# Performance work log

Hardware: AMD Instinct MI355X
Metric: run time of the kernel (lower is better)

## Reference

```python
import jax, jax.numpy as jnp
import numpy as np

BATCH, N_STEPS, STATE_DIM = 8192, 128, 16
HIDDEN = 50
IN0 = STATE_DIM + 1  # features + prev_delta


def _lstm_cell(x, h, c, w_ih, w_hh, b):
    # PyTorch gate order: i, f, g, o
    gates = x @ w_ih.T + h @ w_hh.T + b  # (B, 4H)
    i, f, g, o = jnp.split(gates, 4, axis=-1)
    c_new = jax.nn.sigmoid(f) * c + jax.nn.sigmoid(i) * jnp.tanh(g)
    h_new = jax.nn.sigmoid(o) * jnp.tanh(c_new)
    return h_new, c_new


def setup_inputs() -> dict:
    key = jax.random.key(0)
    ks = jax.random.split(key, 8)
    s = 0.1
    return {
        "features": jax.random.normal(ks[0], (BATCH, N_STEPS, STATE_DIM), dtype=jnp.float32),
        "w_ih0": jax.random.normal(ks[1], (4 * HIDDEN, IN0), dtype=jnp.float32) * s,
        "w_hh0": jax.random.normal(ks[2], (4 * HIDDEN, HIDDEN), dtype=jnp.float32) * s,
        "b_0": jnp.zeros((4 * HIDDEN,), dtype=jnp.float32),  # bias_ih + bias_hh (both init to 0)
        "w_ih1": jax.random.normal(ks[3], (4 * HIDDEN, HIDDEN), dtype=jnp.float32) * s,
        "w_hh1": jax.random.normal(ks[4], (4 * HIDDEN, HIDDEN), dtype=jnp.float32) * s,
        "b_1": jnp.zeros((4 * HIDDEN,), dtype=jnp.float32),
        "w_fc1": jax.random.normal(ks[5], (HIDDEN // 2, HIDDEN), dtype=jnp.float32) * s,
        "b_fc1": jnp.zeros((HIDDEN // 2,), dtype=jnp.float32),
        "w_fc2": jax.random.normal(ks[6], (1, HIDDEN // 2), dtype=jnp.float32) * s,
        "b_fc2": jnp.zeros((1,), dtype=jnp.float32),
    }


def reference(features, w_ih0, w_hh0, b_0, w_ih1, w_hh1, b_1, w_fc1, b_fc1, w_fc2, b_fc2):
    B = features.shape[0]
    feats_t = jnp.swapaxes(features, 0, 1)  # (T, B, state_dim)
    z = jnp.zeros((B, HIDDEN), dtype=features.dtype)
    init = (z, z, z, z, jnp.zeros((B, 1), dtype=features.dtype))

    def step(carry, x_t):
        h0, c0, h1, c1, prev_delta = carry
        x = jnp.concatenate([x_t, prev_delta], axis=-1)  # (B, state_dim+1)
        h0, c0 = _lstm_cell(x, h0, c0, w_ih0, w_hh0, b_0)
        h1, c1 = _lstm_cell(h0, h1, c1, w_ih1, w_hh1, b_1)
        delta = jax.nn.relu(h1 @ w_fc1.T + b_fc1) @ w_fc2.T + b_fc2  # (B, 1)
        return (h0, c0, h1, c1, delta), delta[:, 0]

    _, deltas = jax.lax.scan(step, init, feats_t)  # (T, B)
    return jnp.swapaxes(deltas, 0, 1)  # (B, T)
```

## Files before the change

### kernel.cpp

```cpp
#include <hip/hip_runtime.h>
#include <math.h>

#define BATCH    8192
#define TSTEPS   128
#define SDIM     16
#define HID      50
#define IN0      17
#define BT       16
#define NTHREADS 256

#define K0P 72
#define K1P 104
#define KFP 64

typedef _Float16 half_t;
typedef __attribute__((ext_vector_type(8))) _Float16 half8;
typedef __attribute__((ext_vector_type(4))) float    floatx4;

#define MFMA16(a, b, c) __builtin_amdgcn_mfma_f32_16x16x32_f16((a), (b), (c), 0, 0, 0)

__device__ __forceinline__ float sig_u(float x) {
    float e = __expf(-x);
    return __builtin_amdgcn_rcpf(1.0f + e);
}
__device__ __forceinline__ float tanh_u(float x) {
    float e = __expf(-2.0f * x);
    return fmaf(2.0f, __builtin_amdgcn_rcpf(1.0f + e), -1.0f);
}
__device__ __forceinline__ void hsplit(float v, half_t* hp, half_t* lp) {
    half_t h = (half_t)v;
    *hp = h;
    *lp = (half_t)(v - (float)h);
}

__global__ __launch_bounds__(NTHREADS, 2)
void lstm2_mfma_regw_kernel(const float* __restrict__ feat,
                            const float* __restrict__ w_ih0,
                            const float* __restrict__ w_hh0,
                            const float* __restrict__ b_0,
                            const float* __restrict__ w_ih1,
                            const float* __restrict__ w_hh1,
                            const float* __restrict__ b_1,
                            const float* __restrict__ w_fc1,
                            const float* __restrict__ b_fc1,
                            const float* __restrict__ w_fc2,
                            const float* __restrict__ b_fc2,
                            float* __restrict__ out)
{
    __shared__ __align__(16) half_t smW[200 * K1P];
    __shared__ __align__(16) half_t X0h[BT * K0P], X0l[BT * K0P];
    __shared__ __align__(16) half_t X1h[BT * K1P], X1l[BT * K1P];

    const int tid  = threadIdx.x;
    const int lane = tid & 63;
    const int wv   = tid >> 6;
    const int quad = lane >> 4;
    const int col  = lane & 15;
    const int b0   = blockIdx.x * BT;

    const int tstart = wv * 3 + (wv == 3 ? 1 : 0);
    const int tcnt   = 3 + (wv == 2 ? 1 : 0);

    const half8 hz = {0, 0, 0, 0, 0, 0, 0, 0};


    for (int i = tid; i < 200 * K0P; i += NTHREADS) {
        int row = i / K0P, k = i - row * K0P;
        int j = row >> 2, q = row & 3, orig = q * HID + j;
        float v = 0.0f;
        if (k < IN0)            v = w_ih0[orig * IN0 + k];
        else if (k < IN0 + HID) v = w_hh0[orig * HID + (k - IN0)];
        smW[i] = (half_t)v;
    }
    __syncthreads();
    half8 a0f[3][4];
    #pragma unroll
    for (int kt = 0; kt < 3; ++kt) {
        int k0 = 32 * kt + quad * 8;
        #pragma unroll
        for (int ti = 0; ti < 4; ++ti) {
            a0f[kt][ti] = hz;
            int row = 16 * (tstart + ti) + col;
            if (ti < tcnt && row < 200 && k0 < K0P)
                a0f[kt][ti] = *(const half8*)(smW + row * K0P + k0);
        }
    }
    __syncthreads();

    for (int i = tid; i < 200 * K1P; i += NTHREADS) {
        int row = i / K1P, k = i - row * K1P;
        int j = row >> 2, q = row & 3, orig = q * HID + j;
        float v = 0.0f;
        if (k < HID)                      v = w_hh1[orig * HID + k];
        else if (k >= 52 && k < 52 + HID) v = w_ih1[orig * HID + (k - 52)];
        smW[i] = (half_t)v;
    }
    __syncthreads();
    half8 a1f[4][4];
    #pragma unroll
    for (int kt = 0; kt < 4; ++kt) {
        int k0 = 32 * kt + quad * 8;
        #pragma unroll
        for (int ti = 0; ti < 4; ++ti) {
            a1f[kt][ti] = hz;
            int row = 16 * (tstart + ti) + col;
            if (ti < tcnt && row < 200 && k0 < K1P)
                a1f[kt][ti] = *(const half8*)(smW + row * K1P + k0);
        }
    }
    __syncthreads();

    for (int i = tid; i < 32 * KFP; i += NTHREADS) {
        int row = i >> 6, k = i & 63;
        smW[i] = (half_t)((row < 25 && k < HID) ? w_fc1[row * HID + k] : 0.0f);
    }
    for (int i = tid; i < BT * K0P; i += NTHREADS) { X0h[i] = (half_t)0.0f; X0l[i] = (half_t)0.0f; }
    for (int i = tid; i < BT * K1P; i += NTHREADS) { X1h[i] = (half_t)0.0f; X1l[i] = (half_t)0.0f; }
    __syncthreads();

    half8 wff[2][2];
    wff[0][0] = hz; wff[0][1] = hz; wff[1][0] = hz; wff[1][1] = hz;
    if (wv == 0) {
        #pragma unroll
        for (int kt = 0; kt < 2; ++kt) {
            int k0 = 32 * kt + quad * 8;
            #pragma unroll
            for (int tf = 0; tf < 2; ++tf) {
                int row = 16 * tf + col;
                wff[kt][tf] = *(const half8*)(smW + row * KFP + k0);
            }
        }
    }

    const int xs = tid >> 4, xk = tid & 15;
    const size_t fbase = (size_t)(b0 + xs) * (TSTEPS * SDIM) + xk;
    hsplit(feat[fbase], &X0h[xs * K0P + xk], &X0l[xs * K0P + xk]);

    floatx4 bias0[4], bias1[4];
    #pragma unroll
    for (int ti = 0; ti < 4; ++ti) {
        floatx4 z = {0.f, 0.f, 0.f, 0.f};
        bias0[ti] = z; bias1[ti] = z;
        int u = 4 * (tstart + ti) + quad;
        if (ti < tcnt && u < HID) {
            bias0[ti][0] = b_0[u];           bias0[ti][1] = b_0[HID + u];
            bias0[ti][2] = b_0[2 * HID + u]; bias0[ti][3] = b_0[3 * HID + u];
            bias1[ti][0] = b_1[u];           bias1[ti][1] = b_1[HID + u];
            bias1[ti][2] = b_1[2 * HID + u]; bias1[ti][3] = b_1[3 * HID + u];
        }
    }
    floatx4 w2r[2], bfr[2];
    { floatx4 z = {0.f, 0.f, 0.f, 0.f}; w2r[0] = z; w2r[1] = z; bfr[0] = z; bfr[1] = z; }
    float bf2 = 0.0f;
    if (wv == 0) {
        bf2 = b_fc2[0];
        #pragma unroll
        for (int tf = 0; tf < 2; ++tf)
            #pragma unroll
            for (int r5 = 0; r5 < 4; ++r5) {
                int r = 16 * tf + quad * 4 + r5;
                if (r < 25) { w2r[tf][r5] = w_fc2[r]; bfr[tf][r5] = b_fc1[r]; }
            }
    }

    float c0s[4] = {0.f, 0.f, 0.f, 0.f};
    float c1s[4] = {0.f, 0.f, 0.f, 0.f};
    __syncthreads();

    for (int t = 0; t < TSTEPS; ++t) {
        float fnext = (t + 1 < TSTEPS) ? feat[fbase + (size_t)(t + 1) * SDIM] : 0.0f;

        floatx4 acc[4];
        #pragma unroll
        for (int ti = 0; ti < 4; ++ti) acc[ti] = bias0[ti];
        #pragma unroll
        for (int kt = 0; kt < 3; ++kt) {
            int k0 = 32 * kt + quad * 8;
            half8 bh = hz, bl = hz;
            if (k0 < K0P) {
                bh = *(const half8*)(X0h + col * K0P + k0);
                bl = *(const half8*)(X0l + col * K0P + k0);
            }
            #pragma unroll
            for (int ti = 0; ti < 4; ++ti) {
                if (ti < tcnt) {
                    acc[ti] = MFMA16(a0f[kt][ti], bh, acc[ti]);
                    acc[ti] = MFMA16(a0f[kt][ti], bl, acc[ti]);
                }
            }
        }
        __syncthreads();

        #pragma unroll
        for (int ti = 0; ti < 4; ++ti) {
            if (ti < tcnt) {
                int u = 4 * (tstart + ti) + quad;
                float i_ = sig_u(acc[ti][0]);
                float f_ = sig_u(acc[ti][1]);
                float g_ = tanh_u(acc[ti][2]);
                float o_ = sig_u(acc[ti][3]);
                float c  = f_ * c0s[ti] + i_ * g_;
                c0s[ti]  = c;
                float h  = o_ * tanh_u(c);
                half_t hh, hl;
                hsplit(h, &hh, &hl);
                X1h[col * K1P + 52 + u] = hh;  X1l[col * K1P + 52 + u] = hl;
                X0h[col * K0P + IN0 + u] = hh; X0l[col * K0P + IN0 + u] = hl;
            }
        }
        __syncthreads();

        floatx4 acc1[4];
        #pragma unroll
        for (int ti = 0; ti < 4; ++ti) acc1[ti] = bias1[ti];
        #pragma unroll
        for (int kt = 0; kt < 4; ++kt) {
            int k0 = 32 * kt + quad * 8;
            half8 bh = hz, bl = hz;
            if (k0 < K1P) {
                bh = *(const half8*)(X1h + col * K1P + k0);
                bl = *(const half8*)(X1l + col * K1P + k0);
            }
            #pragma unroll
            for (int ti = 0; ti < 4; ++ti) {
                if (ti < tcnt) {
                    acc1[ti] = MFMA16(a1f[kt][ti], bh, acc1[ti]);
                    acc1[ti] = MFMA16(a1f[kt][ti], bl, acc1[ti]);
                }
            }
        }
        __syncthreads();

        #pragma unroll
        for (int ti = 0; ti < 4; ++ti) {
            if (ti < tcnt) {
                int u = 4 * (tstart + ti) + quad;
                float i_ = sig_u(acc1[ti][0]);
                float f_ = sig_u(acc1[ti][1]);
                float g_ = tanh_u(acc1[ti][2]);
                float o_ = sig_u(acc1[ti][3]);
                float c  = f_ * c1s[ti] + i_ * g_;
                c1s[ti]  = c;
                float h  = o_ * tanh_u(c);
                half_t hh, hl;
                hsplit(h, &hh, &hl);
                X1h[col * K1P + u] = hh;  X1l[col * K1P + u] = hl;
            }
        }
        __syncthreads();

        if (wv == 0) {
            floatx4 accf[2];
            accf[0] = bfr[0]; accf[1] = bfr[1];
            #pragma unroll
            for (int kt = 0; kt < 2; ++kt) {
                int k0 = 32 * kt + quad * 8;
                half8 bh = *(const half8*)(X1h + col * K1P + k0);
                half8 bl = *(const half8*)(X1l + col * K1P + k0);
                #pragma unroll
                for (int tf = 0; tf < 2; ++tf) {
                    accf[tf] = MFMA16(wff[kt][tf], bh, accf[tf]);
                    accf[tf] = MFMA16(wff[kt][tf], bl, accf[tf]);
                }
            }
            float p = 0.0f;
            #pragma unroll
            for (int tf = 0; tf < 2; ++tf)
                #pragma unroll
                for (int r5 = 0; r5 < 4; ++r5)
                    p += w2r[tf][r5] * fmaxf(accf[tf][r5], 0.0f);
            p += __shfl_xor(p, 16);
            p += __shfl_xor(p, 32);
            float d = p + bf2;
            if (lane < 16) {
                out[(size_t)(b0 + lane) * TSTEPS + t] = d;
                hsplit(d, &X0h[lane * K0P + 16], &X0l[lane * K0P + 16]);
            }
        }
        if (t + 1 < TSTEPS)
            hsplit(fnext, &X0h[xs * K0P + xk], &X0l[xs * K0P + xk]);
        __syncthreads();
    }
}

extern "C" void kernel_launch(void* const* d_in, const int* in_sizes, int n_in,
                              void* d_out, int out_size, void* d_ws, size_t ws_size,
                              hipStream_t stream) {
    const float* feat  = (const float*)d_in[0];
    const float* w_ih0 = (const float*)d_in[1];
    const float* w_hh0 = (const float*)d_in[2];
    const float* b_0   = (const float*)d_in[3];
    const float* w_ih1 = (const float*)d_in[4];
    const float* w_hh1 = (const float*)d_in[5];
    const float* b_1   = (const float*)d_in[6];
    const float* w_fc1 = (const float*)d_in[7];
    const float* b_fc1 = (const float*)d_in[8];
    const float* w_fc2 = (const float*)d_in[9];
    const float* b_fc2 = (const float*)d_in[10];
    float* out = (float*)d_out;

    dim3 grid(BATCH / BT);
    dim3 block(NTHREADS);
    hipLaunchKernelGGL(lstm2_mfma_regw_kernel, grid, block, 0, stream,
                       feat, w_ih0, w_hh0, b_0, w_ih1, w_hh1, b_1,
                       w_fc1, b_fc1, w_fc2, b_fc2, out);
}
```

Baseline: 480.1 us.

## Double-buffer LSTM activations, reuse layer-0 h in registers, drop two barriers per step

Replaces the separate X0/X1 activation tiles with one unified, ping-ponged row layout holding features, delta, h0 and h1 at aligned offsets. Each wave now owns a uniform 4 tiles. The h0 fragments loaded for layer 1 are kept in registers and reused for the next step's layer-0 recurrent product. This removes the barriers between each MFMA phase and its gate update, which were needed for in-place overwrites. In exchange it uses more LDS and registers for double buffering and puts weight zero-padding rows into the MFMAs.

```diff
diff --git a/kernel.cpp b/kernel.cpp
--- a/kernel.cpp
+++ b/kernel.cpp
@@ -9,9 +9,12 @@
 #define BT       16
 #define NTHREADS 256
 
-#define K0P 72
-#define K1P 104
-#define KFP 64
+#define RS      160
+#define OFF_H0  32
+#define OFF_H1  96
+#define W0K     96
+#define W1K     128
+#define WFK     64
 
 typedef _Float16 half_t;
 typedef __attribute__((ext_vector_type(8))) _Float16 half8;
@@ -34,115 +37,114 @@
 }
 
 __global__ __launch_bounds__(NTHREADS, 2)
-void lstm2_mfma_regw_kernel(const float* __restrict__ feat,
-                            const float* __restrict__ w_ih0,
-                            const float* __restrict__ w_hh0,
-                            const float* __restrict__ b_0,
-                            const float* __restrict__ w_ih1,
-                            const float* __restrict__ w_hh1,
-                            const float* __restrict__ b_1,
-                            const float* __restrict__ w_fc1,
-                            const float* __restrict__ b_fc1,
-                            const float* __restrict__ w_fc2,
-                            const float* __restrict__ b_fc2,
-                            float* __restrict__ out)
+void lstm2_uni_kernel(const float* __restrict__ feat,
+                      const float* __restrict__ w_ih0,
+                      const float* __restrict__ w_hh0,
+                      const float* __restrict__ b_0,
+                      const float* __restrict__ w_ih1,
+                      const float* __restrict__ w_hh1,
+                      const float* __restrict__ b_1,
+                      const float* __restrict__ w_fc1,
+                      const float* __restrict__ b_fc1,
+                      const float* __restrict__ w_fc2,
+                      const float* __restrict__ b_fc2,
+                      float* __restrict__ out)
 {
-    __shared__ __align__(16) half_t smW[200 * K1P];
-    __shared__ __align__(16) half_t X0h[BT * K0P], X0l[BT * K0P];
-    __shared__ __align__(16) half_t X1h[BT * K1P], X1l[BT * K1P];
+    __shared__ __align__(16) half_t smW[128 * W1K];
+    __shared__ __align__(16) half_t Xh[2][BT * RS];
+    __shared__ __align__(16) half_t Xl[2][BT * RS];
 
     const int tid  = threadIdx.x;
     const int lane = tid & 63;
     const int wv   = tid >> 6;
     const int quad = lane >> 4;
     const int col  = lane & 15;
+    const int k0q  = quad * 8;
     const int b0   = blockIdx.x * BT;
 
-    const int tstart = wv * 3 + (wv == 3 ? 1 : 0);
-    const int tcnt   = 3 + (wv == 2 ? 1 : 0);
+    auto w0val = [&](int r, int k) -> float {
+        if (r >= 200) return 0.0f;
+        int j = r >> 2, q = r & 3, orig = q * HID + j;
+        if (k < IN0) return w_ih0[orig * IN0 + k];
+        if (k < OFF_H0) return 0.0f;
+        int u = k - OFF_H0;
+        return (u < HID) ? w_hh0[orig * HID + u] : 0.0f;
+    };
+    auto w1val = [&](int r, int k) -> float {
+        if (r >= 200) return 0.0f;
+        int j = r >> 2, q = r & 3, orig = q * HID + j;
+        if (k < 64) { return (k < HID) ? w_ih1[orig * HID + k] : 0.0f; }
+        int u = k - 64;
+        return (u < HID) ? w_hh1[orig * HID + u] : 0.0f;
+    };
+
+    const int lrow = 64 * (wv & 1) + col;
+    half8 a0f[3][4], a1f[4][4];
+
+    #pragma unroll 1
+    for (int h = 0; h < 2; ++h) {
+        for (int i = tid; i < 128 * W0K; i += NTHREADS) {
+            int r = i / W0K, kk = i - r * W0K;
+            smW[i] = (half_t)w0val(128 * h + r, kk);
+        }
+        __syncthreads();
+        if ((wv >> 1) == h) {
+            #pragma unroll
+            for (int kt = 0; kt < 3; ++kt)
+                #pragma unroll
+                for (int ti = 0; ti < 4; ++ti)
+                    a0f[kt][ti] = *(const half8*)(smW + (lrow + 16 * ti) * W0K + 32 * kt + k0q);
+        }
+        __syncthreads();
+    }
+    #pragma unroll 1
+    for (int h = 0; h < 2; ++h) {
+        for (int i = tid; i < 128 * W1K; i += NTHREADS) {
+            int r = i >> 7, kk = i & 127;
+            smW[i] = (half_t)w1val(128 * h + r, kk);
+        }
+        __syncthreads();
+        if ((wv >> 1) == h) {
+            #pragma unroll
+            for (int kt = 0; kt < 4; ++kt)
+                #pragma unroll
+                for (int ti = 0; ti < 4; ++ti)
+                    a1f[kt][ti] = *(const half8*)(smW + (lrow + 16 * ti) * W1K + 32 * kt + k0q);
+        }
+        __syncthreads();
+    }
+    for (int i = tid; i < 32 * WFK; i += NTHREADS) {
+        int r = i >> 6, kk = i & 63;
+        smW[i] = (half_t)((r < 25 && kk < HID) ? w_fc1[r * HID + kk] : 0.0f);
+    }
+    for (int i = tid; i < BT * RS; i += NTHREADS) {
+        Xh[0][i] = (half_t)0.0f; Xl[0][i] = (half_t)0.0f;
+        Xh[1][i] = (half_t)0.0f; Xl[1][i] = (half_t)0.0f;
+    }
+    __syncthreads();
 
     const half8 hz = {0, 0, 0, 0, 0, 0, 0, 0};
-
-
-    for (int i = tid; i < 200 * K0P; i += NTHREADS) {
-        int row = i / K0P, k = i - row * K0P;
-        int j = row >> 2, q = row & 3, orig = q * HID + j;
-        float v = 0.0f;
-        if (k < IN0)            v = w_ih0[orig * IN0 + k];
-        else if (k < IN0 + HID) v = w_hh0[orig * HID + (k - IN0)];
-        smW[i] = (half_t)v;
-    }
-    __syncthreads();
-    half8 a0f[3][4];
-    #pragma unroll
-    for (int kt = 0; kt < 3; ++kt) {
-        int k0 = 32 * kt + quad * 8;
-        #pragma unroll
-        for (int ti = 0; ti < 4; ++ti) {
-            a0f[kt][ti] = hz;
-            int row = 16 * (tstart + ti) + col;
-            if (ti < tcnt && row < 200 && k0 < K0P)
-                a0f[kt][ti] = *(const half8*)(smW + row * K0P + k0);
-        }
-    }
-    __syncthreads();
-
-    for (int i = tid; i < 200 * K1P; i += NTHREADS) {
-        int row = i / K1P, k = i - row * K1P;
-        int j = row >> 2, q = row & 3, orig = q * HID + j;
-        float v = 0.0f;
-        if (k < HID)                      v = w_hh1[orig * HID + k];
-        else if (k >= 52 && k < 52 + HID) v = w_ih1[orig * HID + (k - 52)];
-        smW[i] = (half_t)v;
-    }
-    __syncthreads();
-    half8 a1f[4][4];
-    #pragma unroll
-    for (int kt = 0; kt < 4; ++kt) {
-        int k0 = 32 * kt + quad * 8;
-        #pragma unroll
-        for (int ti = 0; ti < 4; ++ti) {
-            a1f[kt][ti] = hz;
-            int row = 16 * (tstart + ti) + col;
-            if (ti < tcnt && row < 200 && k0 < K1P)
-                a1f[kt][ti] = *(const half8*)(smW + row * K1P + k0);
-        }
-    }
-    __syncthreads();
-
-    for (int i = tid; i < 32 * KFP; i += NTHREADS) {
-        int row = i >> 6, k = i & 63;
-        smW[i] = (half_t)((row < 25 && k < HID) ? w_fc1[row * HID + k] : 0.0f);
-    }
-    for (int i = tid; i < BT * K0P; i += NTHREADS) { X0h[i] = (half_t)0.0f; X0l[i] = (half_t)0.0f; }
-    for (int i = tid; i < BT * K1P; i += NTHREADS) { X1h[i] = (half_t)0.0f; X1l[i] = (half_t)0.0f; }
-    __syncthreads();
-
     half8 wff[2][2];
     wff[0][0] = hz; wff[0][1] = hz; wff[1][0] = hz; wff[1][1] = hz;
     if (wv == 0) {
         #pragma unroll
-        for (int kt = 0; kt < 2; ++kt) {
-            int k0 = 32 * kt + quad * 8;
-            #pragma unroll
-            for (int tf = 0; tf < 2; ++tf) {
-                int row = 16 * tf + col;
-                wff[kt][tf] = *(const half8*)(smW + row * KFP + k0);
-            }
-        }
+        for (int kt = 0; kt < 2; ++kt)
+            #pragma unroll
+            for (int tf = 0; tf < 2; ++tf)
+                wff[kt][tf] = *(const half8*)(smW + (16 * tf + col) * WFK + 32 * kt + k0q);
     }
 
     const int xs = tid >> 4, xk = tid & 15;
     const size_t fbase = (size_t)(b0 + xs) * (TSTEPS * SDIM) + xk;
-    hsplit(feat[fbase], &X0h[xs * K0P + xk], &X0l[xs * K0P + xk]);
+    hsplit(feat[fbase], &Xh[0][xs * RS + xk], &Xl[0][xs * RS + xk]);
 
     floatx4 bias0[4], bias1[4];
     #pragma unroll
     for (int ti = 0; ti < 4; ++ti) {
         floatx4 z = {0.f, 0.f, 0.f, 0.f};
         bias0[ti] = z; bias1[ti] = z;
-        int u = 4 * (tstart + ti) + quad;
-        if (ti < tcnt && u < HID) {
+        int u = 4 * (4 * wv + ti) + quad;
+        if (u < HID) {
             bias0[ti][0] = b_0[u];           bias0[ti][1] = b_0[HID + u];
             bias0[ti][2] = b_0[2 * HID + u]; bias0[ti][3] = b_0[3 * HID + u];
             bias1[ti][0] = b_1[u];           bias1[ti][1] = b_1[HID + u];
@@ -165,6 +167,10 @@
 
     float c0s[4] = {0.f, 0.f, 0.f, 0.f};
     float c1s[4] = {0.f, 0.f, 0.f, 0.f};
+    half8 nb1h = hz, nb1l = hz, nb2h = hz, nb2l = hz;
+
+    half_t* Xhc = Xh[0]; half_t* Xlc = Xl[0];
+    half_t* Xhn = Xh[1]; half_t* Xln = Xl[1];
     __syncthreads();
 
     for (int t = 0; t < TSTEPS; ++t) {
@@ -173,90 +179,89 @@
         floatx4 acc[4];
         #pragma unroll
         for (int ti = 0; ti < 4; ++ti) acc[ti] = bias0[ti];
-        #pragma unroll
-        for (int kt = 0; kt < 3; ++kt) {
-            int k0 = 32 * kt + quad * 8;
-            half8 bh = hz, bl = hz;
-            if (k0 < K0P) {
-                bh = *(const half8*)(X0h + col * K0P + k0);
-                bl = *(const half8*)(X0l + col * K0P + k0);
-            }
+        {
+            half8 bh = *(const half8*)(Xhc + col * RS + k0q);
+            half8 bl = *(const half8*)(Xlc + col * RS + k0q);
             #pragma unroll
             for (int ti = 0; ti < 4; ++ti) {
-                if (ti < tcnt) {
-                    acc[ti] = MFMA16(a0f[kt][ti], bh, acc[ti]);
-                    acc[ti] = MFMA16(a0f[kt][ti], bl, acc[ti]);
-                }
-            }
-        }
-        __syncthreads();
-
-        #pragma unroll
-        for (int ti = 0; ti < 4; ++ti) {
-            if (ti < tcnt) {
-                int u = 4 * (tstart + ti) + quad;
-                float i_ = sig_u(acc[ti][0]);
-                float f_ = sig_u(acc[ti][1]);
-                float g_ = tanh_u(acc[ti][2]);
-                float o_ = sig_u(acc[ti][3]);
-                float c  = f_ * c0s[ti] + i_ * g_;
-                c0s[ti]  = c;
-                float h  = o_ * tanh_u(c);
-                half_t hh, hl;
-                hsplit(h, &hh, &hl);
-                X1h[col * K1P + 52 + u] = hh;  X1l[col * K1P + 52 + u] = hl;
-                X0h[col * K0P + IN0 + u] = hh; X0l[col * K0P + IN0 + u] = hl;
-            }
+                acc[ti] = MFMA16(a0f[0][ti], bh, acc[ti]);
+                acc[ti] = MFMA16(a0f[0][ti], bl, acc[ti]);
+            }
+        }
+        #pragma unroll
+        for (int ti = 0; ti < 4; ++ti) {
+            acc[ti] = MFMA16(a0f[1][ti], nb1h, acc[ti]);
+            acc[ti] = MFMA16(a0f[1][ti], nb1l, acc[ti]);
+            acc[ti] = MFMA16(a0f[2][ti], nb2h, acc[ti]);
+            acc[ti] = MFMA16(a0f[2][ti], nb2l, acc[ti]);
+        }
+
+        #pragma unroll
+        for (int ti = 0; ti < 4; ++ti) {
+            int u = 4 * (4 * wv + ti) + quad;
+            float i_ = sig_u(acc[ti][0]);
+            float f_ = sig_u(acc[ti][1]);
+            float g_ = tanh_u(acc[ti][2]);
+            float o_ = sig_u(acc[ti][3]);
+            float c  = f_ * c0s[ti] + i_ * g_;
+            c0s[ti]  = c;
+            float hv = o_ * tanh_u(c);
+            half_t hh, hl; hsplit(hv, &hh, &hl);
+            Xhn[col * RS + OFF_H0 + u] = hh;
+            Xln[col * RS + OFF_H0 + u] = hl;
         }
         __syncthreads();
 
         floatx4 acc1[4];
         #pragma unroll
         for (int ti = 0; ti < 4; ++ti) acc1[ti] = bias1[ti];
-        #pragma unroll
-        for (int kt = 0; kt < 4; ++kt) {
-            int k0 = 32 * kt + quad * 8;
-            half8 bh = hz, bl = hz;
-            if (k0 < K1P) {
-                bh = *(const half8*)(X1h + col * K1P + k0);
-                bl = *(const half8*)(X1l + col * K1P + k0);
-            }
+        nb1h = *(const half8*)(Xhn + col * RS + OFF_H0 + k0q);
+        nb1l = *(const half8*)(Xln + col * RS + OFF_H0 + k0q);
+        #pragma unroll
+        for (int ti = 0; ti < 4; ++ti) {
+            acc1[ti] = MFMA16(a1f[0][ti], nb1h, acc1[ti]);
+            acc1[ti] = MFMA16(a1f[0][ti], nb1l, acc1[ti]);
+        }
+        nb2h = *(const half8*)(Xhn + col * RS + OFF_H0 + 32 + k0q);
+        nb2l = *(const half8*)(Xln + col * RS + OFF_H0 + 32 + k0q);
+        #pragma unroll
+        for (int ti = 0; ti < 4; ++ti) {
+            acc1[ti] = MFMA16(a1f[1][ti], nb2h, acc1[ti]);
+            acc1[ti] = MFMA16(a1f[1][ti], nb2l, acc1[ti]);
+        }
+        #pragma unroll
+        for (int kt = 2; kt < 4; ++kt) {
+            half8 bh = *(const half8*)(Xhc + col * RS + OFF_H1 + 32 * (kt - 2) + k0q);
+            half8 bl = *(const half8*)(Xlc + col * RS + OFF_H1 + 32 * (kt - 2) + k0q);
             #pragma unroll
             for (int ti = 0; ti < 4; ++ti) {
-                if (ti < tcnt) {
-                    acc1[ti] = MFMA16(a1f[kt][ti], bh, acc1[ti]);
-                    acc1[ti] = MFMA16(a1f[kt][ti], bl, acc1[ti]);
-                }
-            }
-        }
-        __syncthreads();
-
-        #pragma unroll
-        for (int ti = 0; ti < 4; ++ti) {
-            if (ti < tcnt) {
-                int u = 4 * (tstart + ti) + quad;
-                float i_ = sig_u(acc1[ti][0]);
-                float f_ = sig_u(acc1[ti][1]);
-                float g_ = tanh_u(acc1[ti][2]);
-                float o_ = sig_u(acc1[ti][3]);
-                float c  = f_ * c1s[ti] + i_ * g_;
-                c1s[ti]  = c;
-                float h  = o_ * tanh_u(c);
-                half_t hh, hl;
-                hsplit(h, &hh, &hl);
-                X1h[col * K1P + u] = hh;  X1l[col * K1P + u] = hl;
-            }
+                acc1[ti] = MFMA16(a1f[kt][ti], bh, acc1[ti]);
+                acc1[ti] = MFMA16(a1f[kt][ti], bl, acc1[ti]);
+            }
+        }
+
+        #pragma unroll
+        for (int ti = 0; ti < 4; ++ti) {
+            int u = 4 * (4 * wv + ti) + quad;
+            float i_ = sig_u(acc1[ti][0]);
+            float f_ = sig_u(acc1[ti][1]);
+            float g_ = tanh_u(acc1[ti][2]);
+            float o_ = sig_u(acc1[ti][3]);
+            float c  = f_ * c1s[ti] + i_ * g_;
+            c1s[ti]  = c;
+            float hv = o_ * tanh_u(c);
+            half_t hh, hl; hsplit(hv, &hh, &hl);
+            Xhn[col * RS + OFF_H1 + u] = hh;
+            Xln[col * RS + OFF_H1 + u] = hl;
         }
         __syncthreads();
 
         if (wv == 0) {
-            floatx4 accf[2];
-            accf[0] = bfr[0]; accf[1] = bfr[1];
+            floatx4 accf[2]; accf[0] = bfr[0]; accf[1] = bfr[1];
             #pragma unroll
             for (int kt = 0; kt < 2; ++kt) {
-                int k0 = 32 * kt + quad * 8;
-                half8 bh = *(const half8*)(X1h + col * K1P + k0);
-                half8 bl = *(const half8*)(X1l + col * K1P + k0);
+                half8 bh = *(const half8*)(Xhn + col * RS + OFF_H1 + 32 * kt + k0q);
+                half8 bl = *(const half8*)(Xln + col * RS + OFF_H1 + 32 * kt + k0q);
                 #pragma unroll
                 for (int tf = 0; tf < 2; ++tf) {
                     accf[tf] = MFMA16(wff[kt][tf], bh, accf[tf]);
@@ -274,12 +279,16 @@
             float d = p + bf2;
             if (lane < 16) {
                 out[(size_t)(b0 + lane) * TSTEPS + t] = d;
-                hsplit(d, &X0h[lane * K0P + 16], &X0l[lane * K0P + 16]);
+                hsplit(d, &Xhn[lane * RS + 16], &Xln[lane * RS + 16]);
             }
         }
         if (t + 1 < TSTEPS)
-            hsplit(fnext, &X0h[xs * K0P + xk], &X0l[xs * K0P + xk]);
-        __syncthreads();
+            hsplit(fnext, &Xhn[xs * RS + xk], &Xln[xs * RS + xk]);
+        __syncthreads();
+
+        half_t* tp;
+        tp = Xhc; Xhc = Xhn; Xhn = tp;
+        tp = Xlc; Xlc = Xln; Xln = tp;
     }
 }
 
@@ -301,7 +310,7 @@
 
     dim3 grid(BATCH / BT);
     dim3 block(NTHREADS);
-    hipLaunchKernelGGL(lstm2_mfma_regw_kernel, grid, block, 0, stream,
+    hipLaunchKernelGGL(lstm2_uni_kernel, grid, block, 0, stream,
                        feat, w_ih0, w_hh0, b_0, w_ih1, w_hh1, b_1,
                        w_fc1, b_fc1, w_fc2, b_fc2, out);
 }
```

Result: no change. 484.8 us (+1.0%).
